# Optimization experiments

Measured on AMD Instinct MI355X. Metric: run time of the kernel, lower is better.

The kernel has to match this reference:

```python
import jax, jax.numpy as jnp
import numpy as np
from jax import lax

B, T = 8, 32
D, H, W = 32, 32, 32
V = D * H * W
NPTS = 400          # nonzero events scattered per frame (<= K)
K = 512             # candidate cap (upper bound on nonzeros per frame)
DIST_THR = 2.0      # distance_threshold
MAX_EVENTS = 100    # max_events


def setup_inputs() -> dict:
    key = jax.random.key(0)
    k1, k2, k3 = jax.random.split(key, 3)
    magnitude = jax.random.normal(k1, (B, T, D, H, W), dtype=jnp.float32)
    # sparse positive energy: scatter NPTS uniform values per frame
    idx = jax.random.randint(k2, (B, T, NPTS), 0, V)
    vals = jax.random.uniform(k3, (B, T, NPTS), minval=0.1, maxval=1.0, dtype=jnp.float32)
    energy = jnp.zeros((B, T, V), jnp.float32).at[
        jnp.arange(B)[:, None, None], jnp.arange(T)[None, :, None], idx
    ].set(vals).reshape(B, T, D, H, W)
    x = jnp.stack([energy, magnitude], axis=2)  # [B,T,2,D,H,W]
    return {"x": x}


def _nms_mask(energy_flat):
    """Greedy 3D NMS over nonzero voxels of one frame. Returns keep-mask over V voxels."""
    scores, idx = lax.top_k(energy_flat, K)          # descending; all nonzeros are in top-K
    valid = scores > 0                               # top_k fill beyond nonzeros has score 0
    z = idx // (H * W)
    y = (idx // W) % H
    xx = idx % W
    coords = jnp.stack([z, y, xx], axis=-1).astype(jnp.float32)  # [K,3]
    ar = jnp.arange(K)

    def body(keep, i):
        active = keep[i] & valid[i]
        dist = jnp.sqrt(((coords[i] - coords) ** 2).sum(-1))
        suppress = active & (ar > i) & (dist < DIST_THR)
        return keep & ~suppress, None

    keep, _ = lax.scan(body, jnp.ones(K, bool), ar)
    keep = keep & valid
    # if more than max_events kept, drop everything past sorted index max_events
    keep = jnp.where(keep.sum() > MAX_EVENTS, keep & (ar < MAX_EVENTS), keep)
    mask = jnp.zeros_like(energy_flat).at[idx].add(keep.astype(energy_flat.dtype))
    return mask  # [V] in {0,1}


def _filter_frame(frame):
    # frame: [2, D, H, W]
    e = frame[0].reshape(V)
    mask = _nms_mask(e).reshape(1, D, H, W)
    has_points = jnp.any(e != 0)
    # empty frame passes through unchanged (original appends x[b,t] as-is)
    return jnp.where(has_points, frame * mask, frame)


def reference(x) -> jnp.ndarray:
    b, t = x.shape[:2]
    frames = x.reshape(b * t, 2, D, H, W)
    out = jax.vmap(_filter_frame)(frames)
    return out.reshape(x.shape)
```

## Files before the change

kernel.cpp:

```cpp
#include <hip/hip_runtime.h>
#include <stdint.h>

typedef unsigned long long u64;
typedef unsigned int u32;

#define VOX     32768
#define KCAP    512
#define MAXEV   100
#define NBRCAP  26
#define NMS_THREADS 1024
#define OUT_THREADS 256
#define CHUNKS  8
#define CHUNK_FLOATS (2 * VOX / CHUNKS)
#define MAXSURV 128

struct Surv { int vox; float val; };


__global__ __launch_bounds__(NMS_THREADS) void nms_kernel(
    const float* __restrict__ x, int* __restrict__ nsurv, Surv* __restrict__ surv)
{
    const int f   = blockIdx.x;
    const int tid = threadIdx.x;
    const float* __restrict__ e = x + (size_t)f * 2 * VOX;

    __shared__ unsigned short smap[VOX];
    __shared__ u64   skey[KCAP];
    __shared__ short srank[KCAP];
    __shared__ unsigned char status[KCAP];
    __shared__ unsigned short pnbr[KCAP * NBRCAP];
    __shared__ int s_cntpos, s_cntnz, s_nkept, s_out, s_undec;

    if (tid == 0) { s_cntpos = 0; s_cntnz = 0; s_nkept = 0; s_out = 0; }
    {
        u32* m32 = (u32*)smap;
        #pragma unroll
        for (int h = 0; h < VOX / 2 / NMS_THREADS; ++h)
            m32[tid + h * NMS_THREADS] = 0xFFFFFFFFu;
    }
    __syncthreads();

    {
        const float4* e4 = (const float4*)e;
        int nzloc = 0;
        #pragma unroll
        for (int h = 0; h < VOX / 4 / NMS_THREADS; ++h) {
            int i = tid + h * NMS_THREADS;
            float4 v = e4[i];
            float vv[4] = {v.x, v.y, v.z, v.w};
            #pragma unroll
            for (int c = 0; c < 4; ++c) {
                float val = vv[c];
                if (val > 0.f) {
                    nzloc++;
                    int slot = atomicAdd(&s_cntpos, 1);
                    if (slot < KCAP) {
                        int vox = i * 4 + c;
                        skey[slot] = ((u64)__float_as_uint(val) << 32) | (u64)(~(u32)vox);
                        smap[vox]  = (unsigned short)slot;
                    }
                } else if (val != 0.f) {
                    nzloc++;
                }
            }
        }
        if (nzloc) atomicAdd(&s_cntnz, nzloc);
    }
    __syncthreads();

    const int npos  = min(s_cntpos, KCAP);
    const int anynz = s_cntnz;

    int pcnt = 0;
    if (tid < npos) {
        const u64 kt = skey[tid];

        int rank = 0;
        #pragma unroll 8
        for (int i = 0; i < npos; ++i)
            rank += (skey[i] > kt);
        srank[tid] = (short)rank;

        const int vox = (int)(~(u32)kt) & (VOX - 1);
        const int zt = vox >> 10, yt = (vox >> 5) & 31, xt = vox & 31;
        #pragma unroll
        for (int dz = -1; dz <= 1; ++dz) {
            int z = zt + dz; if ((unsigned)z >= 32) continue;
            #pragma unroll
            for (int dy = -1; dy <= 1; ++dy) {
                int yy = yt + dy; if ((unsigned)yy >= 32) continue;
                #pragma unroll
                for (int dx = -1; dx <= 1; ++dx) {
                    int xx = xt + dx; if ((unsigned)xx >= 32) continue;
                    int nv = (z << 10) | (yy << 5) | xx;
                    if (nv == vox) continue;
                    unsigned short m = smap[nv];
                    if (m != 0xFFFFu && skey[m] > kt)
                        pnbr[tid * NBRCAP + pcnt++] = m;
                }
            }
        }
        status[tid] = (pcnt == 0) ? (unsigned char)1 : (unsigned char)0;
    }
    __syncthreads();

    for (int round = 0; round < KCAP; ++round) {
        if (tid == 0) s_undec = 0;
        __syncthreads();
        if (tid < npos && status[tid] == 0) {
            bool anyKept = false, anyUndec = false;
            for (int p = 0; p < pcnt; ++p) {
                unsigned char s = status[pnbr[tid * NBRCAP + p]];
                anyKept  |= (s == 1);
                anyUndec |= (s == 0);
            }
            if (anyKept)        status[tid] = 2;
            else if (!anyUndec) status[tid] = 1;
            else                s_undec = 1;
        }
        __syncthreads();
        if (s_undec == 0) break;
    }

    if (tid < npos && status[tid] == 1) atomicAdd(&s_nkept, 1);
    __syncthreads();
    const int nkept = s_nkept;
    if (tid < npos && status[tid] == 1 &&
        !(nkept > MAXEV && srank[tid] >= MAXEV)) {
        int slot = atomicAdd(&s_out, 1);
        u64 kt = skey[tid];
        Surv s;
        s.vox = (int)(~(u32)kt) & (VOX - 1);
        s.val = __uint_as_float((u32)(kt >> 32));
        surv[f * MAXSURV + slot] = s;
    }
    __syncthreads();
    if (tid == 0) nsurv[f] = anynz ? s_out : -1;
}

__global__ __launch_bounds__(OUT_THREADS) void output_kernel(
    const float* __restrict__ x, const int* __restrict__ nsurv,
    const Surv* __restrict__ surv, float* __restrict__ out)
{
    const int bid = blockIdx.x;
    const int f   = bid / CHUNKS;
    const int c   = bid % CHUNKS;
    const int tid = threadIdx.x;

    const float* __restrict__ xf = x   + (size_t)f * 2 * VOX;
    float*       __restrict__ of = out + (size_t)f * 2 * VOX;
    const int base = c * CHUNK_FLOATS;
    const int ns   = nsurv[f];

    if (ns < 0) {
        const float4* x4 = (const float4*)(xf + base);
        float4*       o4 = (float4*)(of + base);
        #pragma unroll
        for (int h = 0; h < CHUNK_FLOATS / 4 / OUT_THREADS; ++h)
            o4[tid + h * OUT_THREADS] = x4[tid + h * OUT_THREADS];
        return;
    }

    {
        float4* o4 = (float4*)(of + base);
        const float4 z = make_float4(0.f, 0.f, 0.f, 0.f);
        #pragma unroll
        for (int h = 0; h < CHUNK_FLOATS / 4 / OUT_THREADS; ++h)
            o4[tid + h * OUT_THREADS] = z;
    }
    __syncthreads();

    if (tid < ns) {
        Surv s = surv[f * MAXSURV + tid];
        int vox = s.vox;
        int ec  = vox >> 13;
        if (c == ec) {
            of[vox] = s.val;
        } else if (c == ec + CHUNKS / 2) {
            of[VOX + vox] = xf[VOX + vox];
        }
    }
}

extern "C" void kernel_launch(void* const* d_in, const int* in_sizes, int n_in,
                              void* d_out, int out_size, void* d_ws, size_t ws_size,
                              hipStream_t stream) {
    const float* x = (const float*)d_in[0];
    float* out = (float*)d_out;
    int frames = in_sizes[0] / (2 * VOX);

    int*  nsurv = (int*)d_ws;
    Surv* surv  = (Surv*)((char*)d_ws + 4096);

    nms_kernel<<<frames, NMS_THREADS, 0, stream>>>(x, nsurv, surv);
    output_kernel<<<frames * CHUNKS, OUT_THREADS, 0, stream>>>(x, nsurv, surv, out);
}
```

Baseline: 129.7 us.

## Split energy scan across blocks per frame and fuse scatter into NMS kernel

The energy scan and candidate compaction move out of the single-block-per-frame NMS kernel into a multi-block staging kernel. It uses wave-level ballot plus one global atomic per wavefront and also zero-fills the output. The NMS kernel then loads the compacted candidates from global memory and writes survivors directly to the output, removing the separate output pass. The aim is to spread the memory-bound scan over many more blocks and to cut one full output write pass. The cost is a memset, global atomics, and a scatter that depends on the earlier zero-fill. Candidate order now depends on global atomic ordering, but ranks come from the key comparison, so results stay deterministic.

```diff
diff --git a/kernel.cpp b/kernel.cpp
--- a/kernel.cpp
+++ b/kernel.cpp
@@ -8,76 +8,109 @@
 #define KCAP    512
 #define MAXEV   100
 #define NBRCAP  26
-#define NMS_THREADS 1024
-#define OUT_THREADS 256
-#define CHUNKS  8
-#define CHUNK_FLOATS (2 * VOX / CHUNKS)
-#define MAXSURV 128
-
-struct Surv { int vox; float val; };
+#define K1_BPF  8
+#define K1_THREADS 256
+#define K2_THREADS 512
 
 
-__global__ __launch_bounds__(NMS_THREADS) void nms_kernel(
-    const float* __restrict__ x, int* __restrict__ nsurv, Surv* __restrict__ surv)
+__global__ __launch_bounds__(K1_THREADS) void stage_kernel(
+    const float* __restrict__ x, float* __restrict__ out,
+    int* __restrict__ gcnt, int* __restrict__ gnz, u64* __restrict__ grec)
+{
+    const int bid  = blockIdx.x;
+    const int f    = bid / K1_BPF;
+    const int c    = bid % K1_BPF;
+    const int tid  = threadIdx.x;
+    const int lane = tid & 63;
+
+    {
+        float4* o4 = (float4*)(out + (size_t)f * 2 * VOX) + c * (2 * VOX / K1_BPF / 4);
+        const float4 z = make_float4(0.f, 0.f, 0.f, 0.f);
+        #pragma unroll
+        for (int h = 0; h < (2 * VOX / K1_BPF / 4) / K1_THREADS; ++h)
+            o4[tid + h * K1_THREADS] = z;
+    }
+
+    const float4* e4 = (const float4*)(x + (size_t)f * 2 * VOX) + c * (VOX / K1_BPF / 4);
+    bool anynz = false;
+    #pragma unroll
+    for (int h = 0; h < (VOX / K1_BPF / 4) / K1_THREADS; ++h) {
+        int li = tid + h * K1_THREADS;
+        float4 v = e4[li];
+        int vbase = c * (VOX / K1_BPF) + li * 4;
+        float vv[4] = {v.x, v.y, v.z, v.w};
+        #pragma unroll
+        for (int cc = 0; cc < 4; ++cc) {
+            float val = vv[cc];
+            anynz |= (val != 0.f);
+            bool pos = (val > 0.f);
+            u64 m = __ballot(pos);
+            if (m) {
+                int leader = __ffsll(m) - 1;
+                int base;
+                if (lane == leader) base = atomicAdd(&gcnt[f], __popcll(m));
+                base = __shfl(base, leader);
+                if (pos) {
+                    int off = base + __popcll(m & ((1ull << lane) - 1ull));
+                    if (off < KCAP) {
+                        int vox = vbase + cc;
+                        grec[f * KCAP + off] =
+                            ((u64)__float_as_uint(val) << 32) | (u64)(~(u32)vox);
+                    }
+                }
+            }
+        }
+    }
+    if (__ballot(anynz) && lane == 0) gnz[f] = 1;
+}
+
+__global__ __launch_bounds__(K2_THREADS) void nms_scatter_kernel(
+    const float* __restrict__ x, float* __restrict__ out,
+    const int* __restrict__ gcnt, const int* __restrict__ gnz,
+    const u64* __restrict__ grec)
 {
     const int f   = blockIdx.x;
     const int tid = threadIdx.x;
-    const float* __restrict__ e = x + (size_t)f * 2 * VOX;
 
     __shared__ unsigned short smap[VOX];
     __shared__ u64   skey[KCAP];
     __shared__ short srank[KCAP];
     __shared__ unsigned char status[KCAP];
     __shared__ unsigned short pnbr[KCAP * NBRCAP];
-    __shared__ int s_cntpos, s_cntnz, s_nkept, s_out, s_undec;
+    __shared__ int s_nkept, s_undec;
 
-    if (tid == 0) { s_cntpos = 0; s_cntnz = 0; s_nkept = 0; s_out = 0; }
+    const int n  = min(gcnt[f], KCAP);
+    const int nz = gnz[f];
+
+    if (nz == 0) {
+        const float4* x4 = (const float4*)(x + (size_t)f * 2 * VOX);
+        float4*       o4 = (float4*)(out + (size_t)f * 2 * VOX);
+        for (int i = tid; i < 2 * VOX / 4; i += K2_THREADS) o4[i] = x4[i];
+        return;
+    }
+
+    if (tid == 0) s_nkept = 0;
     {
         u32* m32 = (u32*)smap;
         #pragma unroll
-        for (int h = 0; h < VOX / 2 / NMS_THREADS; ++h)
-            m32[tid + h * NMS_THREADS] = 0xFFFFFFFFu;
+        for (int h = 0; h < VOX / 2 / K2_THREADS; ++h)
+            m32[tid + h * K2_THREADS] = 0xFFFFFFFFu;
     }
     __syncthreads();
 
-    {
-        const float4* e4 = (const float4*)e;
-        int nzloc = 0;
-        #pragma unroll
-        for (int h = 0; h < VOX / 4 / NMS_THREADS; ++h) {
-            int i = tid + h * NMS_THREADS;
-            float4 v = e4[i];
-            float vv[4] = {v.x, v.y, v.z, v.w};
-            #pragma unroll
-            for (int c = 0; c < 4; ++c) {
-                float val = vv[c];
-                if (val > 0.f) {
-                    nzloc++;
-                    int slot = atomicAdd(&s_cntpos, 1);
-                    if (slot < KCAP) {
-                        int vox = i * 4 + c;
-                        skey[slot] = ((u64)__float_as_uint(val) << 32) | (u64)(~(u32)vox);
-                        smap[vox]  = (unsigned short)slot;
-                    }
-                } else if (val != 0.f) {
-                    nzloc++;
-                }
-            }
-        }
-        if (nzloc) atomicAdd(&s_cntnz, nzloc);
+    if (tid < n) {
+        u64 k = grec[f * KCAP + tid];
+        skey[tid] = k;
+        smap[(int)(~(u32)k) & (VOX - 1)] = (unsigned short)tid;
     }
     __syncthreads();
 
-    const int npos  = min(s_cntpos, KCAP);
-    const int anynz = s_cntnz;
-
     int pcnt = 0;
-    if (tid < npos) {
+    if (tid < n) {
         const u64 kt = skey[tid];
-
         int rank = 0;
         #pragma unroll 8
-        for (int i = 0; i < npos; ++i)
+        for (int i = 0; i < n; ++i)
             rank += (skey[i] > kt);
         srank[tid] = (short)rank;
 
@@ -107,7 +140,7 @@
     for (int round = 0; round < KCAP; ++round) {
         if (tid == 0) s_undec = 0;
         __syncthreads();
-        if (tid < npos && status[tid] == 0) {
+        if (tid < n && status[tid] == 0) {
             bool anyKept = false, anyUndec = false;
             for (int p = 0; p < pcnt; ++p) {
                 unsigned char s = status[pnbr[tid * NBRCAP + p]];
@@ -122,63 +155,17 @@
         if (s_undec == 0) break;
     }
 
-    if (tid < npos && status[tid] == 1) atomicAdd(&s_nkept, 1);
+    if (tid < n && status[tid] == 1) atomicAdd(&s_nkept, 1);
     __syncthreads();
     const int nkept = s_nkept;
-    if (tid < npos && status[tid] == 1 &&
+    if (tid < n && status[tid] == 1 &&
         !(nkept > MAXEV && srank[tid] >= MAXEV)) {
-        int slot = atomicAdd(&s_out, 1);
-        u64 kt = skey[tid];
-        Surv s;
-        s.vox = (int)(~(u32)kt) & (VOX - 1);
-        s.val = __uint_as_float((u32)(kt >> 32));
-        surv[f * MAXSURV + slot] = s;
-    }
-    __syncthreads();
-    if (tid == 0) nsurv[f] = anynz ? s_out : -1;
-}
-
-__global__ __launch_bounds__(OUT_THREADS) void output_kernel(
-    const float* __restrict__ x, const int* __restrict__ nsurv,
-    const Surv* __restrict__ surv, float* __restrict__ out)
-{
-    const int bid = blockIdx.x;
-    const int f   = bid / CHUNKS;
-    const int c   = bid % CHUNKS;
-    const int tid = threadIdx.x;
-
-    const float* __restrict__ xf = x   + (size_t)f * 2 * VOX;
-    float*       __restrict__ of = out + (size_t)f * 2 * VOX;
-    const int base = c * CHUNK_FLOATS;
-    const int ns   = nsurv[f];
-
-    if (ns < 0) {
-        const float4* x4 = (const float4*)(xf + base);
-        float4*       o4 = (float4*)(of + base);
-        #pragma unroll
-        for (int h = 0; h < CHUNK_FLOATS / 4 / OUT_THREADS; ++h)
-            o4[tid + h * OUT_THREADS] = x4[tid + h * OUT_THREADS];
-        return;
-    }
-
-    {
-        float4* o4 = (float4*)(of + base);
-        const float4 z = make_float4(0.f, 0.f, 0.f, 0.f);
-        #pragma unroll
-        for (int h = 0; h < CHUNK_FLOATS / 4 / OUT_THREADS; ++h)
-            o4[tid + h * OUT_THREADS] = z;
-    }
-    __syncthreads();
-
-    if (tid < ns) {
-        Surv s = surv[f * MAXSURV + tid];
-        int vox = s.vox;
-        int ec  = vox >> 13;
-        if (c == ec) {
-            of[vox] = s.val;
-        } else if (c == ec + CHUNKS / 2) {
-            of[VOX + vox] = xf[VOX + vox];
-        }
+        u64 k = skey[tid];
+        int   vox = (int)(~(u32)k) & (VOX - 1);
+        float val = __uint_as_float((u32)(k >> 32));
+        float* of = out + (size_t)f * 2 * VOX;
+        of[vox]       = val;
+        of[VOX + vox] = x[(size_t)f * 2 * VOX + VOX + vox];
     }
 }
 
@@ -189,9 +176,11 @@
     float* out = (float*)d_out;
     int frames = in_sizes[0] / (2 * VOX);
 
-    int*  nsurv = (int*)d_ws;
-    Surv* surv  = (Surv*)((char*)d_ws + 4096);
+    int* gcnt = (int*)d_ws;
+    int* gnz  = (int*)((char*)d_ws + 1024);
+    u64* grec = (u64*)((char*)d_ws + 4096);
 
-    nms_kernel<<<frames, NMS_THREADS, 0, stream>>>(x, nsurv, surv);
-    output_kernel<<<frames * CHUNKS, OUT_THREADS, 0, stream>>>(x, nsurv, surv, out);
+    hipMemsetAsync(d_ws, 0, 2048, stream);
+    stage_kernel<<<frames * K1_BPF, K1_THREADS, 0, stream>>>(x, out, gcnt, gnz, grec);
+    nms_scatter_kernel<<<frames, K2_THREADS, 0, stream>>>(x, out, gcnt, gnz, grec);
 }
```

Result: slower. 236.5 us (+82.3%).
